# Performance work log

Hardware: AMD Instinct MI355X
Metric: run time of the kernel (lower is better)

Reference implementation:

```python
import jax, jax.numpy as jnp
import numpy as np

N, D, E, K = 65536, 2048, 64, 8
EPS = 1e-5


def setup_inputs() -> dict:
    key = jax.random.key(0)
    kx, kw = jax.random.split(key)
    x = jax.random.normal(kx, (N, D), dtype=jnp.float32)
    # nn.Linear(input_size, num_experts, bias=False) weight: [E, D]
    W = jax.random.normal(kw, (E, D), dtype=jnp.float32) * (1.0 / np.sqrt(D))
    return {"x": x, "W": W}


def _l1_normalize(v):
    # torch F.normalize(p=1, dim=0): v / max(||v||_1, 1e-12)
    return v / jnp.maximum(jnp.sum(jnp.abs(v)), 1e-12)


def reference(x, W):
    # router logits: [N, E] in float32 (matches .float() in torch code)
    logits = (x @ W.T).astype(jnp.float32)
    top_v, top_i = jax.lax.top_k(logits, K)            # [N, K]
    top_k_gates = jax.nn.softmax(top_v, axis=-1).astype(x.dtype)
    # training-branch aux loss (compute_aux_loss)
    probs = jax.nn.softmax(logits, axis=-1)            # [N, E]
    rows = jnp.arange(logits.shape[0])[:, None]
    dense_gates = jnp.zeros_like(probs, dtype=top_k_gates.dtype).at[rows, top_i].set(top_k_gates)
    probs_sum = probs.sum(0)                           # [E]
    freq = (dense_gates > 0).astype(jnp.float32).sum(0)  # [E]
    # log(sum(exp(logits)) + eps)^2 summed, computed stably
    lse = jnp.logaddexp(jax.scipy.special.logsumexp(logits, axis=-1), jnp.log(EPS))
    zloss = jnp.sum(lse ** 2) / logits.shape[0]
    switchloss = E * jnp.sum(_l1_normalize(probs_sum) * _l1_normalize(freq))
    loss = switchloss + 0.1 * zloss
    return top_i, top_k_gates, loss
```

## Files before the change

### kernel.cpp

```cpp
#include <hip/hip_runtime.h>
#include <math.h>

#define NROWS 65536
#define DDIM 2048
#define NEXP 64
#define TOPK 8

constexpr int NSTEP = 64;
constexpr float THR = 3e-4f;
constexpr int WFRAG_STEP = 4096;

typedef short bf16x8 __attribute__((ext_vector_type(8)));
typedef float f32x4 __attribute__((ext_vector_type(4)));

__device__ inline unsigned short bfround(float f) {
    union { float f; unsigned u; } v; v.f = f;
    unsigned r = (v.u + 0x7fffu + ((v.u >> 16) & 1u)) >> 16;
    return (unsigned short)r;
}
__device__ inline float bf2f(unsigned short h) {
    union { unsigned u; float f; } v; v.u = ((unsigned)h) << 16;
    return v.f;
}
__device__ inline void cvt8(const float4& A, const float4& B, bf16x8& h, bf16x8& l) {
    float f[8] = {A.x, A.y, A.z, A.w, B.x, B.y, B.z, B.w};
#pragma unroll
    for (int j = 0; j < 8; ++j) {
        unsigned short hh = bfround(f[j]);
        h[j] = (short)hh;
        l[j] = (short)bfround(f[j] - bf2f(hh));
    }
}

__global__ __launch_bounds__(256)
void prep_kernel(const float* __restrict__ W, short* __restrict__ wfrag)
{
    const int t = blockIdx.x;
    const int tid = threadIdx.x;
    const int ct = tid >> 6, lane = tid & 63;
    const int e = ct * 16 + (lane & 15);
    const int k = t * 32 + (lane >> 4) * 8;
    const float* wp = W + (size_t)e * DDIM + k;
    float4 a = *reinterpret_cast<const float4*>(wp);
    float4 b = *reinterpret_cast<const float4*>(wp + 4);
    bf16x8 h, l;
    cvt8(a, b, h, l);
    short* base = wfrag + (size_t)t * WFRAG_STEP;
    *reinterpret_cast<bf16x8*>(base + (ct * 64 + lane) * 8) = h;
    *reinterpret_cast<bf16x8*>(base + 2048 + (ct * 64 + lane) * 8) = l;
}

__global__ __launch_bounds__(256, 2)
void gemm_kernel(const float* __restrict__ x, const short* __restrict__ wfrag,
                 float* __restrict__ logits)
{
    __shared__ __align__(16) short Bfrag[2][2][4][64][8];

    const int tid = threadIdx.x;
    const int w = tid >> 6;
    const int lane = tid & 63;
    const int g = lane >> 4;
    const int c = lane & 15;
    const int row0 = blockIdx.x * 64 + w * 16;
    const float* xr = x + (size_t)(row0 + c) * DDIM + g * 8;

    const int se = tid >> 2, skg = tid & 3;
    const int sct = se >> 4;
    const int slane = (se & 15) + (skg << 4);
    const int soff = (sct * 64 + slane) * 8;

    auto stageB = [&](int t, int buf) {
        const short* src = wfrag + (size_t)t * WFRAG_STEP + soff;
        *reinterpret_cast<bf16x8*>(&Bfrag[buf][0][sct][slane][0]) =
            *reinterpret_cast<const bf16x8*>(src);
        *reinterpret_cast<bf16x8*>(&Bfrag[buf][1][sct][slane][0]) =
            *reinterpret_cast<const bf16x8*>(src + 2048);
    };

    f32x4 acc[4];
#pragma unroll
    for (int ct = 0; ct < 4; ++ct) acc[ct] = (f32x4){0.f, 0.f, 0.f, 0.f};

    float4 xa0 = *reinterpret_cast<const float4*>(xr);
    float4 xa1 = *reinterpret_cast<const float4*>(xr + 4);
    float4 xb0, xb1;
    stageB(0, 0);
    __syncthreads();

    for (int t = 0; t < NSTEP; ++t) {
        const int buf = t & 1;
        const int kn = (t + 1) * 32;
        if (t + 1 < NSTEP) {
            xb0 = *reinterpret_cast<const float4*>(xr + kn);
            xb1 = *reinterpret_cast<const float4*>(xr + kn + 4);
            stageB(t + 1, buf ^ 1);
        }
        bf16x8 ah, al;
        cvt8(xa0, xa1, ah, al);
#pragma unroll
        for (int ct = 0; ct < 4; ++ct) {
            bf16x8 bh = *reinterpret_cast<const bf16x8*>(&Bfrag[buf][0][ct][lane][0]);
            bf16x8 bl = *reinterpret_cast<const bf16x8*>(&Bfrag[buf][1][ct][lane][0]);
            acc[ct] = __builtin_amdgcn_mfma_f32_16x16x32_bf16(ah, bh, acc[ct], 0, 0, 0);
            acc[ct] = __builtin_amdgcn_mfma_f32_16x16x32_bf16(ah, bl, acc[ct], 0, 0, 0);
            acc[ct] = __builtin_amdgcn_mfma_f32_16x16x32_bf16(al, bh, acc[ct], 0, 0, 0);
        }
        xa0 = xb0; xa1 = xb1;
        __syncthreads();
    }

#pragma unroll
    for (int ct = 0; ct < 4; ++ct)
#pragma unroll
        for (int reg = 0; reg < 4; ++reg)
            logits[(size_t)(row0 + g * 4 + reg) * NEXP + ct * 16 + c] = acc[ct][reg];
}

__global__ __launch_bounds__(256, 2)
void epilogue_kernel(const float* __restrict__ x, const float* __restrict__ W,
                     const float* __restrict__ logits,
                     float* __restrict__ out_idx, float* __restrict__ out_gate,
                     float* __restrict__ g_psum, float* __restrict__ g_freq,
                     float* __restrict__ g_zsum)
{
    __shared__ float psum_s[NEXP];
    __shared__ float fcnt_s[NEXP];
    __shared__ float zsq_s;
    __shared__ int fList[4][8];
    __shared__ int fN[4];
    const int tid = threadIdx.x;
    const int w = tid >> 6;
    const int lane = tid & 63;
    const int g = lane >> 4;
    const int c = lane & 15;
    if (tid < NEXP) { psum_s[tid] = 0.f; fcnt_s[tid] = 0.f; }
    if (tid == 0) zsq_s = 0.f;
    if (lane == 0) fN[w] = 0;
    __syncthreads();

    const int wi = blockIdx.x * 4 + w;
    float pcol[4] = {0.f, 0.f, 0.f, 0.f};
    float zacc = 0.f;

    for (int it = 0; it < 2; ++it) {
        const int row = wi * 8 + it * 4 + g;
        float4 Lv = *reinterpret_cast<const float4*>(&logits[(size_t)row * NEXP + c * 4]);
        float L[4] = {Lv.x, Lv.y, Lv.z, Lv.w};
        float ld[4] = {L[0], L[1], L[2], L[3]};

        float tv[9]; int ti[9];
#pragma unroll
        for (int p = 0; p < 9; ++p) {
            float bv = -3.4e38f; int bgi = 127;
#pragma unroll
            for (int j = 0; j < 4; ++j) {
                int e = c * 4 + j;
                if (ld[j] > bv) { bv = ld[j]; bgi = e; }
            }
#pragma unroll
            for (int m = 1; m < 16; m <<= 1) {
                float ov = __shfl_xor(bv, m, 16);
                int ogi = __shfl_xor(bgi, m, 16);
                if (ov > bv || (ov == bv && ogi < bgi)) { bv = ov; bgi = ogi; }
            }
            tv[p] = bv; ti[p] = bgi;
#pragma unroll
            for (int j = 0; j < 4; ++j)
                if (bgi == c * 4 + j) ld[j] = -3.4e38f;
        }

        const float m0 = tv[0];
        float pe[4], ps = 0.f;
#pragma unroll
        for (int j = 0; j < 4; ++j) { pe[j] = expf(L[j] - m0); ps += pe[j]; }
        float s = ps;
#pragma unroll
        for (int m = 1; m < 16; m <<= 1) s += __shfl_xor(s, m, 16);
        const float inv_s = 1.f / s;
#pragma unroll
        for (int j = 0; j < 4; ++j) pcol[j] += pe[j] * inv_s;

        if (c == 0) {
            float lsef = m0 + logf(s);
            const float lb = -11.512925464970229f;
            float mx = fmaxf(lsef, lb), mn = fminf(lsef, lb);
            float z = mx + log1pf(expf(mn - mx));
            zacc += z * z;
        }

        float mg = 3.4e38f;
#pragma unroll
        for (int p = 0; p < 8; ++p) mg = fminf(mg, tv[p] - tv[p + 1]);
        const bool flagged = (mg < THR);
        const size_t base = (size_t)row * TOPK;

        float gs = 0.f;
#pragma unroll
        for (int p = 0; p < 8; ++p) gs += expf(tv[p] - m0);
        if (c < 8) {
            float mytv = tv[0]; int myti = ti[0];
#pragma unroll
            for (int p = 1; p < 8; ++p)
                if (c == p) { mytv = tv[p]; myti = ti[p]; }
            out_idx[base + c] = (float)myti;
            out_gate[base + c] = expf(mytv - m0) / gs;
            if (!flagged) atomicAdd(&fcnt_s[myti], 1.f);
        }
        if (flagged && c == 0) {
            int sl = atomicAdd(&fN[w], 1);
            fList[w][sl] = row;
        }
    }

    const int nf = fN[w];
    for (int si = 0; si < nf; ++si) {
        const int row = fList[w][si];
        const float lg = logits[(size_t)row * NEXP + lane];

        unsigned u = __float_as_uint(lg);
        unsigned ordb = (u & 0x80000000u) ? ~u : (u | 0x80000000u);
        unsigned long long key =
            ((unsigned long long)ordb << 32) | (unsigned)(63 - lane);
#pragma unroll
        for (int k = 2; k <= 64; k <<= 1) {
#pragma unroll
            for (int j = k >> 1; j > 0; j >>= 1) {
                unsigned long long other = __shfl_xor(key, j, 64);
                const bool keep_max = ((lane & j) == 0) == ((lane & k) == 0);
                const bool mine_bigger = key > other;
                key = (keep_max == mine_bigger) ? key : other;
            }
        }
        unsigned ou = (unsigned)(key >> 32);
        unsigned ub = (ou & 0x80000000u) ? (ou ^ 0x80000000u) : ~ou;
        const float val = __uint_as_float(ub);
        const float v9 = __shfl(val, 8, 64);

        const bool cand = (lg >= v9 - THR);
        unsigned long long cm = __ballot(cand);
        const float* xrw = x + (size_t)row * DDIM;
        float4 xv[8];
#pragma unroll
        for (int j = 0; j < 8; ++j)
            xv[j] = *reinterpret_cast<const float4*>(xrw + j * 256 + lane * 4);

        double myD = -HUGE_VAL;
        unsigned long long m2 = cm;
        while (m2) {
            const int e = (int)__ffsll((unsigned long long)m2) - 1;
            m2 &= (m2 - 1);
            const float* wrp = W + (size_t)e * DDIM;
            double p0 = 0.0, p1 = 0.0, p2 = 0.0, p3 = 0.0;
#pragma unroll
            for (int j = 0; j < 8; ++j) {
                float4 wv = *reinterpret_cast<const float4*>(wrp + j * 256 + lane * 4);
                p0 = fma((double)xv[j].x, (double)wv.x, p0);
                p1 = fma((double)xv[j].y, (double)wv.y, p1);
                p2 = fma((double)xv[j].z, (double)wv.z, p2);
                p3 = fma((double)xv[j].w, (double)wv.w, p3);
            }
            double sd = (p0 + p1) + (p2 + p3);
#pragma unroll
            for (int m = 1; m < 64; m <<= 1) sd += __shfl_xor(sd, m, 64);
            if (lane == e) myD = sd;
        }

        double v = cand ? myD : -HUGE_VAL;
        double tvd[8]; int ti8[8];
#pragma unroll
        for (int p = 0; p < 8; ++p) {
            double bv = v; int bgi = lane;
#pragma unroll
            for (int m = 1; m < 64; m <<= 1) {
                double ov = __shfl_xor(bv, m, 64);
                int ogi = __shfl_xor(bgi, m, 64);
                if (ov > bv || (ov == bv && ogi < bgi)) { bv = ov; bgi = ogi; }
            }
            tvd[p] = bv; ti8[p] = bgi;
            if (lane == bgi) v = -HUGE_VAL;
        }
        const double m0d = tvd[0];
        double gsum = 0.0, ge[8];
#pragma unroll
        for (int j = 0; j < 8; ++j) { ge[j] = exp(tvd[j] - m0d); gsum += ge[j]; }
        if (lane < 8) {
            double myge = ge[0]; int myti = ti8[0];
#pragma unroll
            for (int j = 1; j < 8; ++j)
                if (lane == j) { myge = ge[j]; myti = ti8[j]; }
            const size_t base = (size_t)row * TOPK;
            out_idx[base + lane] = (float)myti;
            out_gate[base + lane] = (float)(myge / gsum);
            atomicAdd(&fcnt_s[myti], 1.f);
        }
    }

#pragma unroll
    for (int j = 0; j < 4; ++j) atomicAdd(&psum_s[c * 4 + j], pcol[j]);
    if (c == 0) atomicAdd(&zsq_s, zacc);
    __syncthreads();
    if (tid < NEXP) {
        atomicAdd(&g_psum[tid], psum_s[tid]);
        atomicAdd(&g_freq[tid], fcnt_s[tid]);
    }
    if (tid == 0) atomicAdd(g_zsum, zsq_s);
}

__global__ void finalize_kernel(const float* __restrict__ g_psum,
                                const float* __restrict__ g_freq,
                                const float* __restrict__ g_zsum,
                                float* __restrict__ out_loss)
{
    const int lane = threadIdx.x & 63;
    float p = g_psum[lane], f = g_freq[lane];
    float sp = p, sf = f;
#pragma unroll
    for (int m = 1; m < 64; m <<= 1) { sp += __shfl_xor(sp, m, 64); sf += __shfl_xor(sf, m, 64); }
    sp = fmaxf(sp, 1e-12f);
    sf = fmaxf(sf, 1e-12f);
    float term = (p / sp) * (f / sf);
#pragma unroll
    for (int m = 1; m < 64; m <<= 1) term += __shfl_xor(term, m, 64);
    if (lane == 0)
        out_loss[0] = (float)NEXP * term + 0.1f * (g_zsum[0] / (float)NROWS);
}

extern "C" void kernel_launch(void* const* d_in, const int* in_sizes, int n_in,
                              void* d_out, int out_size, void* d_ws, size_t ws_size,
                              hipStream_t stream)
{
    const float* x = (const float*)d_in[0];
    const float* W = (const float*)d_in[1];
    float* out = (float*)d_out;
    float* out_idx  = out;
    float* out_gate = out + (size_t)NROWS * TOPK;
    float* out_loss = out + (size_t)2 * NROWS * TOPK;

    float* acc    = (float*)d_ws;
    float* logits = (float*)d_ws + 256;
    short* wfrag  = (short*)((float*)d_ws + 256 + (size_t)NROWS * NEXP);
    hipMemsetAsync(d_ws, 0, 129 * sizeof(float), stream);

    prep_kernel<<<NSTEP, 256, 0, stream>>>(W, wfrag);
    gemm_kernel<<<NROWS / 64, 256, 0, stream>>>(x, wfrag, logits);
    epilogue_kernel<<<2048, 256, 0, stream>>>(x, W, logits, out_idx, out_gate,
                                              acc, acc + NEXP, acc + 2 * NEXP);
    finalize_kernel<<<1, 64, 0, stream>>>(acc, acc + NEXP, acc + 2 * NEXP, out_loss);
}
```

Baseline: 264.7 us.

## Move near-tie top-k recheck into a separate globally load-balanced fixup kernel

```diff
diff --git a/kernel.cpp b/kernel.cpp
--- a/kernel.cpp
+++ b/kernel.cpp
@@ -9,6 +9,7 @@
 constexpr int NSTEP = 64;
 constexpr float THR = 3e-4f;
 constexpr int WFRAG_STEP = 4096;
+constexpr int CAP = 16384;
 
 typedef short bf16x8 __attribute__((ext_vector_type(8)));
 typedef float f32x4 __attribute__((ext_vector_type(4)));
@@ -117,17 +118,15 @@
 }
 
 __global__ __launch_bounds__(256, 2)
-void epilogue_kernel(const float* __restrict__ x, const float* __restrict__ W,
-                     const float* __restrict__ logits,
+void epilogue_kernel(const float* __restrict__ logits,
                      float* __restrict__ out_idx, float* __restrict__ out_gate,
                      float* __restrict__ g_psum, float* __restrict__ g_freq,
-                     float* __restrict__ g_zsum)
+                     float* __restrict__ g_zsum, int* __restrict__ g_cnt,
+                     int* __restrict__ g_rows)
 {
     __shared__ float psum_s[NEXP];
     __shared__ float fcnt_s[NEXP];
     __shared__ float zsq_s;
-    __shared__ int fList[4][8];
-    __shared__ int fN[4];
     const int tid = threadIdx.x;
     const int w = tid >> 6;
     const int lane = tid & 63;
@@ -135,7 +134,6 @@
     const int c = lane & 15;
     if (tid < NEXP) { psum_s[tid] = 0.f; fcnt_s[tid] = 0.f; }
     if (tid == 0) zsq_s = 0.f;
-    if (lane == 0) fN[w] = 0;
     __syncthreads();
 
     const int wi = blockIdx.x * 4 + w;
@@ -172,7 +170,7 @@
         const float m0 = tv[0];
         float pe[4], ps = 0.f;
 #pragma unroll
-        for (int j = 0; j < 4; ++j) { pe[j] = expf(L[j] - m0); ps += pe[j]; }
+        for (int j = 0; j < 4; ++j) { pe[j] = __expf(L[j] - m0); ps += pe[j]; }
         float s = ps;
 #pragma unroll
         for (int m = 1; m < 16; m <<= 1) s += __shfl_xor(s, m, 16);
@@ -181,10 +179,10 @@
         for (int j = 0; j < 4; ++j) pcol[j] += pe[j] * inv_s;
 
         if (c == 0) {
-            float lsef = m0 + logf(s);
+            float lsef = m0 + __logf(s);
             const float lb = -11.512925464970229f;
             float mx = fmaxf(lsef, lb), mn = fminf(lsef, lb);
-            float z = mx + log1pf(expf(mn - mx));
+            float z = mx + log1pf(__expf(mn - mx));
             zacc += z * z;
         }
 
@@ -196,25 +194,47 @@
 
         float gs = 0.f;
 #pragma unroll
-        for (int p = 0; p < 8; ++p) gs += expf(tv[p] - m0);
+        for (int p = 0; p < 8; ++p) gs += __expf(tv[p] - m0);
         if (c < 8) {
             float mytv = tv[0]; int myti = ti[0];
 #pragma unroll
             for (int p = 1; p < 8; ++p)
                 if (c == p) { mytv = tv[p]; myti = ti[p]; }
             out_idx[base + c] = (float)myti;
-            out_gate[base + c] = expf(mytv - m0) / gs;
+            out_gate[base + c] = __expf(mytv - m0) / gs;
             if (!flagged) atomicAdd(&fcnt_s[myti], 1.f);
         }
         if (flagged && c == 0) {
-            int sl = atomicAdd(&fN[w], 1);
-            fList[w][sl] = row;
-        }
-    }
-
-    const int nf = fN[w];
-    for (int si = 0; si < nf; ++si) {
-        const int row = fList[w][si];
+            int idx = atomicAdd(g_cnt, 1);
+            if (idx < CAP) g_rows[idx] = row;
+        }
+    }
+
+#pragma unroll
+    for (int j = 0; j < 4; ++j) atomicAdd(&psum_s[c * 4 + j], pcol[j]);
+    if (c == 0) atomicAdd(&zsq_s, zacc);
+    __syncthreads();
+    if (tid < NEXP) {
+        atomicAdd(&g_psum[tid], psum_s[tid]);
+        atomicAdd(&g_freq[tid], fcnt_s[tid]);
+    }
+    if (tid == 0) atomicAdd(g_zsum, zsq_s);
+}
+
+__global__ __launch_bounds__(256, 1)
+void fixup_kernel(const float* __restrict__ x, const float* __restrict__ W,
+                  const float* __restrict__ logits,
+                  float* __restrict__ out_idx, float* __restrict__ out_gate,
+                  float* __restrict__ g_freq,
+                  const int* __restrict__ g_cnt, const int* __restrict__ g_rows)
+{
+    const int n = min(*g_cnt, CAP);
+    const int lane = threadIdx.x & 63;
+    const int wid = (blockIdx.x * blockDim.x + threadIdx.x) >> 6;
+    const int nw = (gridDim.x * blockDim.x) >> 6;
+
+    for (int i = wid; i < n; i += nw) {
+        const int row = g_rows[i];
         const float lg = logits[(size_t)row * NEXP + lane];
 
         unsigned u = __float_as_uint(lg);
@@ -291,19 +311,9 @@
             const size_t base = (size_t)row * TOPK;
             out_idx[base + lane] = (float)myti;
             out_gate[base + lane] = (float)(myge / gsum);
-            atomicAdd(&fcnt_s[myti], 1.f);
-        }
-    }
-
-#pragma unroll
-    for (int j = 0; j < 4; ++j) atomicAdd(&psum_s[c * 4 + j], pcol[j]);
-    if (c == 0) atomicAdd(&zsq_s, zacc);
-    __syncthreads();
-    if (tid < NEXP) {
-        atomicAdd(&g_psum[tid], psum_s[tid]);
-        atomicAdd(&g_freq[tid], fcnt_s[tid]);
-    }
-    if (tid == 0) atomicAdd(g_zsum, zsq_s);
+            atomicAdd(&g_freq[myti], 1.0f);
+        }
+    }
 }
 
 __global__ void finalize_kernel(const float* __restrict__ g_psum,
@@ -337,13 +347,18 @@
     float* out_loss = out + (size_t)2 * NROWS * TOPK;
 
     float* acc    = (float*)d_ws;
-    float* logits = (float*)d_ws + 256;
-    short* wfrag  = (short*)((float*)d_ws + 256 + (size_t)NROWS * NEXP);
-    hipMemsetAsync(d_ws, 0, 129 * sizeof(float), stream);
+    int*   cnt    = (int*)d_ws + 129;
+    int*   rows   = (int*)d_ws + 130;
+    float* logits = (float*)d_ws + 32768;
+    short* wfrag  = (short*)((float*)d_ws + 32768 + (size_t)NROWS * NEXP);
+    hipMemsetAsync(d_ws, 0, 132 * sizeof(float), stream);
 
     prep_kernel<<<NSTEP, 256, 0, stream>>>(W, wfrag);
     gemm_kernel<<<NROWS / 64, 256, 0, stream>>>(x, wfrag, logits);
-    epilogue_kernel<<<2048, 256, 0, stream>>>(x, W, logits, out_idx, out_gate,
-                                              acc, acc + NEXP, acc + 2 * NEXP);
+    epilogue_kernel<<<2048, 256, 0, stream>>>(logits, out_idx, out_gate,
+                                              acc, acc + NEXP, acc + 2 * NEXP,
+                                              cnt, rows);
+    fixup_kernel<<<512, 256, 0, stream>>>(x, W, logits, out_idx, out_gate,
+                                          acc + NEXP, cnt, rows);
     finalize_kernel<<<1, 64, 0, stream>>>(acc, acc + NEXP, acc + 2 * NEXP, out_loss);
 }
```

After: 280.2 us. 1.06x slower.
